# Optimization experiments

Hardware: AMD Instinct MI355X
Metric: run time of the kernel (lower is better)

## Reference

```python
import jax, jax.numpy as jnp
import numpy as np
import math

S, E, D, H = 2048, 1024, 64, 16  # seq, embedding_dim (=D*H), per-head d_model, heads


def setup_inputs() -> dict:
    ks = jax.random.split(jax.random.key(0), 14)
    u = lambda k, sh: jax.random.uniform(k, sh, dtype=jnp.float32)
    n = lambda k, sh, s=0.02: s * jax.random.normal(k, sh, dtype=jnp.float32)
    return {
        "x": jax.random.normal(ks[0], (S, E), dtype=jnp.float32),
        # nn.Parameter(torch.rand(d_model, embedding_dim))
        "Wk": u(ks[1], (D, E)),
        "Wq": u(ks[2], (D, E)),
        "Wv": u(ks[3], (D, E)),
        # per-head Linear(d_model, d_model): weight [out,in]=[D,D], bias [D]
        "hWk": n(ks[4], (H, D, D)), "hbk": n(ks[5], (H, D)),
        "hWv": n(ks[6], (H, D, D)), "hbv": n(ks[7], (H, D)),
        "hWq": n(ks[8], (H, D, D)), "hbq": n(ks[9], (H, D)),
        # last_linear: Linear(D*H, D*H)
        "Wo": n(ks[10], (E, E)), "bo": n(ks[11], (E,)),
        # LayerNorm(D*H)
        "gamma": jnp.ones((E,), jnp.float32),
        "beta": jnp.zeros((E,), jnp.float32),
    }


def reference(x, Wk, Wq, Wv, hWk, hbk, hWv, hbv, hWq, hbq, Wo, bo, gamma, beta):
    # shared projections: [S, E] @ [E, D] -> [S, D]
    K = x @ Wk.T
    Q = x @ Wq.T
    V = x @ Wv.T
    # per-head linears (torch Linear: y = x @ W.T + b), vectorized over heads
    Kh = jnp.einsum('sd,hed->hse', K, hWk) + hbk[:, None, :]  # [H, S, D]
    Vh = jnp.einsum('sd,hed->hse', V, hWv) + hbv[:, None, :]
    Qh = jnp.einsum('sd,hed->hse', Q, hWq) + hbq[:, None, :]
    # scaled dot product attention; scale uses sqrt(d_model)
    scores = jnp.einsum('hqd,hkd->hqk', Qh, Kh) / math.sqrt(D)  # [H, S, S]
    attn = jax.nn.softmax(scores, axis=-1)
    O = jnp.einsum('hqk,hkd->hqd', attn, Vh)  # [H, S, D]
    # concat heads along feature dim (head order) -> [S, H*D]
    cat = jnp.transpose(O, (1, 0, 2)).reshape(S, H * D)
    out = cat @ Wo.T + bo
    # residual + LayerNorm (eps 1e-5)
    y = out + x
    mu = jnp.mean(y, axis=-1, keepdims=True)
    var = jnp.mean(jnp.square(y - mu), axis=-1, keepdims=True)
    return (y - mu) * jax.lax.rsqrt(var + 1e-5) * gamma + beta
```

## Files before the change

kernel.cpp:

```cpp
#include <hip/hip_runtime.h>
#include <math.h>

#define S 2048
#define E 1024
#define D 64
#define H 16

using f16 = _Float16;
typedef _Float16 v8h __attribute__((ext_vector_type(8)));
typedef _Float16 v4h __attribute__((ext_vector_type(4)));
typedef _Float16 v2h __attribute__((ext_vector_type(2)));
typedef float v4f __attribute__((ext_vector_type(4)));

__device__ __forceinline__ float fexp2(float x) { return __builtin_amdgcn_exp2f(x); }

__device__ __forceinline__ void glds16(const f16* g, f16* l) {
    __builtin_amdgcn_global_load_lds(
        (const __attribute__((address_space(1))) void*)g,
        (__attribute__((address_space(3))) void*)l, 16, 0, 0);
}

__global__ void convert_all(const float* __restrict__ x, const float* __restrict__ Wo,
                            f16* __restrict__ Xh, f16* __restrict__ WoB) {
    const size_t i = (size_t)blockIdx.x * 256 + threadIdx.x;
    const size_t NX = (size_t)S * E / 4;
    if (i < NX) {
        v4f w = ((const v4f*)x)[i];
        v4h h = {(f16)w[0], (f16)w[1], (f16)w[2], (f16)w[3]};
        ((v4h*)Xh)[i] = h;
    } else {
        const size_t j = i - NX;
        v4f w = ((const v4f*)Wo)[j];
        v4h h = {(f16)w[0], (f16)w[1], (f16)w[2], (f16)w[3]};
        ((v4h*)WoB)[j] = h;
    }
}

__global__ void wprep(const float* __restrict__ hWk, const float* __restrict__ hWq,
                      const float* __restrict__ hWv,
                      const float* __restrict__ Wk, const float* __restrict__ Wq,
                      const float* __restrict__ Wv,
                      f16* __restrict__ Wc) {
    const int th = blockIdx.x;
    const int type = th >> 4, h = th & 15;
    const int e0 = blockIdx.y * 64;
    const float* hW = ((type == 0) ? hWk : (type == 1) ? hWq : hWv) + (size_t)h * D * D;
    const float* W  = (type == 0) ? Wk : (type == 1) ? Wq : Wv;
    const int t = threadIdx.x;

    __shared__ f16 Ah[64][72];
    __shared__ f16 Bt[64][72];

    {
        const int r16 = t >> 4, c4 = (t & 15) * 4;
#pragma unroll
        for (int rep = 0; rep < 4; ++rep) {
            const int row = rep * 16 + r16;
            v4f a = *(const v4f*)&hW[(size_t)row * D + c4];
#pragma unroll
            for (int j = 0; j < 4; ++j) Ah[row][c4 + j] = (f16)a[j];
            v4f w = *(const v4f*)&W[(size_t)row * E + e0 + c4];
#pragma unroll
            for (int j = 0; j < 4; ++j) Bt[c4 + j][row] = (f16)w[j];
        }
    }
    __syncthreads();

    const int wave = t >> 6, lane = t & 63;
    const int quad = lane >> 4, l16 = lane & 15;
    v4f acc[4] = {{0,0,0,0},{0,0,0,0},{0,0,0,0},{0,0,0,0}};
#pragma unroll
    for (int ks = 0; ks < 2; ++ks) {
        v8h af = *(const v8h*)&Ah[wave * 16 + l16][ks * 32 + quad * 8];
#pragma unroll
        for (int nt = 0; nt < 4; ++nt) {
            v8h bf = *(const v8h*)&Bt[nt * 16 + l16][ks * 32 + quad * 8];
            acc[nt] = __builtin_amdgcn_mfma_f32_16x16x32_f16(af, bf, acc[nt], 0, 0, 0);
        }
    }
#pragma unroll
    for (int r = 0; r < 4; ++r) {
        const int e2 = wave * 16 + quad * 4 + r;
#pragma unroll
        for (int nt = 0; nt < 4; ++nt)
            Wc[((size_t)th * D + e2) * E + e0 + nt * 16 + l16] = (f16)acc[nt][r];
    }
}

__global__ __launch_bounds__(256) void qkv_gemm(
        const f16* __restrict__ Xh, const f16* __restrict__ Wc,
        const float* __restrict__ hbk, const float* __restrict__ hbq,
        const float* __restrict__ hbv,
        f16* __restrict__ Kh, f16* __restrict__ Qh, f16* __restrict__ Vh) {
    const int m0 = blockIdx.x * 128;
    const int n0 = blockIdx.y * 64;
    const int type = n0 >> 10, h = (n0 >> 6) & 15;
    const float* hb = ((type == 0) ? hbk : (type == 1) ? hbq : hbv) + h * D;
    f16* outp = (type == 0) ? Kh : (type == 1) ? Qh : Vh;

    const int t = threadIdx.x;
    const int wave = t >> 6, lane = t & 63;
    const int quad = lane >> 4, l16 = lane & 15;
    const int wm = wave >> 1, wn = wave & 1;

    __shared__ f16 As[128 * 64];
    __shared__ f16 Bs[64 * 64];

    v4f acc[4][2] = {};
    const int lrow8 = lane >> 3, lg = lane & 7;

    for (int k0 = 0; k0 < E; k0 += 64) {
        __syncthreads();
#pragma unroll
        for (int jj = 0; jj < 4; ++jj) {
            const int j = wave * 4 + jj;
            const int row = j * 8 + lrow8;
            const int g = lg ^ (row & 7);
            glds16(Xh + (size_t)(m0 + row) * E + k0 + g * 8, &As[j * 512]);
        }
#pragma unroll
        for (int jj = 0; jj < 2; ++jj) {
            const int j = wave * 2 + jj;
            const int row = j * 8 + lrow8;
            const int g = lg ^ (row & 7);
            glds16(Wc + (size_t)(n0 + row) * E + k0 + g * 8, &Bs[j * 512]);
        }
        __syncthreads();

#pragma unroll
        for (int ks = 0; ks < 2; ++ks) {
            v8h a[4], b[2];
#pragma unroll
            for (int mt = 0; mt < 4; ++mt) {
                const int row = wm * 64 + mt * 16 + l16;
                a[mt] = *(const v8h*)&As[row * 64 + (((ks * 4 + quad) ^ (row & 7)) * 8)];
            }
#pragma unroll
            for (int nt = 0; nt < 2; ++nt) {
                const int row = wn * 32 + nt * 16 + l16;
                b[nt] = *(const v8h*)&Bs[row * 64 + (((ks * 4 + quad) ^ (row & 7)) * 8)];
            }
#pragma unroll
            for (int mt = 0; mt < 4; ++mt)
#pragma unroll
                for (int nt = 0; nt < 2; ++nt)
                    acc[mt][nt] = __builtin_amdgcn_mfma_f32_16x16x32_f16(a[mt], b[nt], acc[mt][nt], 0, 0, 0);
        }
    }

#pragma unroll
    for (int mt = 0; mt < 4; ++mt)
#pragma unroll
        for (int r = 0; r < 4; ++r) {
            const int s = m0 + wm * 64 + mt * 16 + quad * 4 + r;
#pragma unroll
            for (int nt = 0; nt < 2; ++nt) {
                const int d = wn * 32 + nt * 16 + l16;
                outp[((size_t)h * S + s) * D + d] = (f16)(acc[mt][nt][r] + hb[d]);
            }
        }
}

__global__ void v_transpose(const f16* __restrict__ Vh, f16* __restrict__ VhT) {
    const int h = blockIdx.x;
    const int s0 = blockIdx.y * 64;
    const int t = threadIdx.x;

    __shared__ f16 T[64][66];

    {
        const int r = t >> 2, c = (t & 3) * 16;
        v8h a = *(const v8h*)(Vh + ((size_t)h * S + s0 + r) * D + c);
        v8h b = *(const v8h*)(Vh + ((size_t)h * S + s0 + r) * D + c + 8);
#pragma unroll
        for (int j = 0; j < 8; ++j) { T[r][c + j] = a[j]; T[r][c + 8 + j] = b[j]; }
    }
    __syncthreads();
    {
        const int d = t >> 2, sc = (t & 3) * 16;
        v8h a, b;
#pragma unroll
        for (int j = 0; j < 8; ++j) { a[j] = T[sc + j][d]; b[j] = T[sc + 8 + j][d]; }
        f16* o = VhT + ((size_t)h * D + d) * S + s0 + sc;
        *(v8h*)o = a;
        *(v8h*)(o + 8) = b;
    }
}

#define NSPLIT 4
#define KSPAN (S / NSPLIT)
#define ITERS (KSPAN / 64)
#define PPAD 72

__global__ __launch_bounds__(256, 5) void attn_mfma(
        const f16* __restrict__ Qh, const f16* __restrict__ Kh,
        const f16* __restrict__ VhT, f16* __restrict__ Opart,
        float* __restrict__ ml) {
    const int h = blockIdx.y;
    const int q0 = blockIdx.x * 64;
    const int sp = blockIdx.z;
    const int t = threadIdx.x;
    const int wave = t >> 6, lane = t & 63;
    const int quad = lane >> 4, l16 = lane & 15;

    __shared__ f16 Kt[64 * 64];
    __shared__ f16 Vt[80 * 64];
    __shared__ union { f16 P[4][16][PPAD]; f16 O[64][PPAD]; } PO;

    {
        v4h one = {(f16)1, (f16)1, (f16)1, (f16)1};
        *(v4h*)&Vt[64 * 64 + t * 4] = one;
    }

    const int qrow = q0 + wave * 16 + l16;
    v8h qf[2];
    {
        const v8h* qp = (const v8h*)(Qh + ((size_t)h * S + qrow) * D);
        qf[0] = qp[quad];
        qf[1] = qp[quad + 4];
    }

    v4f oc[5] = {};
    float m_run = -INFINITY;
    const float scale = 0.125f * 1.44269504f;
    const int kb = sp * KSPAN;
    const int srow = lane >> 3, sg = lane & 7;

    for (int it = 0; it < ITERS; ++it) {
        __syncthreads();
#pragma unroll
        for (int half = 0; half < 2; ++half) {
            const int row = wave * 16 + half * 8 + srow;
            const int g = sg ^ (row & 7);
            glds16(Kh + ((size_t)h * S + kb + it * 64 + row) * D + g * 8,
                   &Kt[(wave * 16 + half * 8) * 64]);
            glds16(VhT + ((size_t)h * D + row) * S + kb + it * 64 + g * 8,
                   &Vt[(wave * 16 + half * 8) * 64]);
        }
        __syncthreads();

        v4f sc[4] = {};
#pragma unroll
        for (int ks = 0; ks < 2; ++ks)
#pragma unroll
            for (int mt = 0; mt < 4; ++mt) {
                const int key = mt * 16 + l16;
                v8h kf = *(const v8h*)&Kt[key * 64 + (((ks * 4 + quad) ^ (key & 7)) * 8)];
                sc[mt] = __builtin_amdgcn_mfma_f32_16x16x32_f16(kf, qf[ks], sc[mt], 0, 0, 0);
            }

        float v = sc[0][0];
#pragma unroll
        for (int mt = 0; mt < 4; ++mt)
#pragma unroll
            for (int r = 0; r < 4; ++r) v = fmaxf(v, sc[mt][r]);
        v = fmaxf(v, __shfl_xor(v, 16));
        v = fmaxf(v, __shfl_xor(v, 32));
        v *= scale;
        const float mnew = fmaxf(m_run, v);
        const float alpha = fexp2(m_run - mnew);
        m_run = mnew;
#pragma unroll
        for (int i = 0; i < 5; ++i) oc[i] *= alpha;

#pragma unroll
        for (int mt = 0; mt < 4; ++mt) {
            const float p0 = fexp2(fmaf(sc[mt][0], scale, -mnew));
            const float p1 = fexp2(fmaf(sc[mt][1], scale, -mnew));
            const float p2 = fexp2(fmaf(sc[mt][2], scale, -mnew));
            const float p3 = fexp2(fmaf(sc[mt][3], scale, -mnew));
            auto lo = __builtin_amdgcn_cvt_pkrtz(p0, p1);
            auto hi = __builtin_amdgcn_cvt_pkrtz(p2, p3);
            v4h ph; ph[0] = lo[0]; ph[1] = lo[1]; ph[2] = hi[0]; ph[3] = hi[1];
            *(v4h*)&PO.P[wave][l16][mt * 16 + quad * 4] = ph;
        }

#pragma unroll
        for (int ks = 0; ks < 2; ++ks) {
            v8h pf = *(const v8h*)&PO.P[wave][l16][ks * 32 + quad * 8];
#pragma unroll
            for (int mt = 0; mt < 5; ++mt) {
                const int dr = mt * 16 + l16;
                v8h vf = *(const v8h*)&Vt[dr * 64 + (((ks * 4 + quad) ^ (dr & 7)) * 8)];
                oc[mt] = __builtin_amdgcn_mfma_f32_16x16x32_f16(vf, pf, oc[mt], 0, 0, 0);
            }
        }
    }

    const float l = oc[4][0];
    const float invl = 1.f / l;
    __syncthreads();
#pragma unroll
    for (int mt = 0; mt < 4; ++mt) {
        auto lo = __builtin_amdgcn_cvt_pkrtz(oc[mt][0] * invl, oc[mt][1] * invl);
        auto hi = __builtin_amdgcn_cvt_pkrtz(oc[mt][2] * invl, oc[mt][3] * invl);
        v4h oh; oh[0] = lo[0]; oh[1] = lo[1]; oh[2] = hi[0]; oh[3] = hi[1];
        *(v4h*)&PO.O[wave * 16 + l16][mt * 16 + quad * 4] = oh;
    }
    if (quad == 0) {
        float* mlp = ml + (((size_t)sp * H + h) * S + qrow) * 2;
        mlp[0] = m_run;
        mlp[1] = l;
    }
    __syncthreads();
    {
        const int q = t >> 2, dg = (t & 3) * 16;
        v8h o0 = *(const v8h*)&PO.O[q][dg];
        v8h o1 = *(const v8h*)&PO.O[q][dg + 8];
        f16* dst = Opart + (((size_t)sp * H + h) * S + q0 + q) * D + dg;
        *(v8h*)dst = o0;
        *(v8h*)(dst + 8) = o1;
    }
}

__global__ void attn_combine(const f16* __restrict__ Opart,
                             const float* __restrict__ ml,
                             f16* __restrict__ cat) {
    const int q = blockIdx.x;
    const int t = threadIdx.x;
#pragma unroll
    for (int i = 0; i < 4; ++i) {
        const int idx = i * 256 + t;
        const int h = idx >> 6, d = idx & 63;
        float m[NSPLIT], lv[NSPLIT];
        float M = -INFINITY;
#pragma unroll
        for (int sp = 0; sp < NSPLIT; ++sp) {
            const float* mlp = ml + (((size_t)sp * H + h) * S + q) * 2;
            m[sp] = mlp[0]; lv[sp] = mlp[1];
            M = fmaxf(M, m[sp]);
        }
        float asum = 0.f, o = 0.f;
#pragma unroll
        for (int sp = 0; sp < NSPLIT; ++sp) {
            const float a = fexp2(m[sp] - M) * lv[sp];
            asum += a;
            o += a * (float)Opart[(((size_t)sp * H + h) * S + q) * D + d];
        }
        cat[(size_t)q * E + h * D + d] = (f16)(o / asum);
    }
}

__global__ __launch_bounds__(256) void gemm_y(
        const f16* __restrict__ cat, const f16* __restrict__ WoB,
        const float* __restrict__ bo, const float* __restrict__ x,
        float* __restrict__ y) {
    const int m0 = blockIdx.x * 64;
    const int n0 = blockIdx.y * 64;
    const int t = threadIdx.x;
    const int wave = t >> 6, lane = t & 63;
    const int quad = lane >> 4, l16 = lane & 15;
    const int wm = wave >> 1, wn = wave & 1;

    __shared__ f16 As[64 * 64];
    __shared__ f16 Bs[64 * 64];

    v4f acc[2][2] = {};
    const int lrow8 = lane >> 3, lg = lane & 7;

    for (int k0 = 0; k0 < E; k0 += 64) {
        __syncthreads();
#pragma unroll
        for (int jj = 0; jj < 2; ++jj) {
            const int j = wave * 2 + jj;
            const int row = j * 8 + lrow8;
            const int g = lg ^ (row & 7);
            glds16(cat + (size_t)(m0 + row) * E + k0 + g * 8, &As[j * 512]);
            glds16(WoB + (size_t)(n0 + row) * E + k0 + g * 8, &Bs[j * 512]);
        }
        __syncthreads();

#pragma unroll
        for (int ks = 0; ks < 2; ++ks) {
            v8h a[2], b[2];
#pragma unroll
            for (int mt = 0; mt < 2; ++mt) {
                const int row = wm * 32 + mt * 16 + l16;
                a[mt] = *(const v8h*)&As[row * 64 + (((ks * 4 + quad) ^ (row & 7)) * 8)];
            }
#pragma unroll
            for (int nt = 0; nt < 2; ++nt) {
                const int row = wn * 32 + nt * 16 + l16;
                b[nt] = *(const v8h*)&Bs[row * 64 + (((ks * 4 + quad) ^ (row & 7)) * 8)];
            }
#pragma unroll
            for (int mt = 0; mt < 2; ++mt)
#pragma unroll
                for (int nt = 0; nt < 2; ++nt)
                    acc[mt][nt] = __builtin_amdgcn_mfma_f32_16x16x32_f16(a[mt], b[nt], acc[mt][nt], 0, 0, 0);
        }
    }

#pragma unroll
    for (int mt = 0; mt < 2; ++mt)
#pragma unroll
        for (int r = 0; r < 4; ++r) {
            const int m = m0 + wm * 32 + mt * 16 + quad * 4 + r;
#pragma unroll
            for (int nt = 0; nt < 2; ++nt) {
                const int e = n0 + wn * 32 + nt * 16 + l16;
                y[(size_t)m * E + e] = acc[mt][nt][r] + bo[e] + x[(size_t)m * E + e];
            }
        }
}

__global__ void ln(const float* __restrict__ y,
                   const float* __restrict__ gamma,
                   const float* __restrict__ beta,
                   float* __restrict__ out) {
    const int s = blockIdx.x;
    const int t = threadIdx.x;
    __shared__ float red[256];

    v4f yv = *(const v4f*)(y + (size_t)s * E + t * 4);
    red[t] = yv[0] + yv[1] + yv[2] + yv[3];
    __syncthreads();
    for (int w = 128; w > 0; w >>= 1) {
        if (t < w) red[t] += red[t + w];
        __syncthreads();
    }
    const float mu = red[0] * (1.f / E);
    __syncthreads();

    float lv = 0.f;
#pragma unroll
    for (int i = 0; i < 4; ++i) { float dd = yv[i] - mu; lv += dd * dd; }
    red[t] = lv;
    __syncthreads();
    for (int w = 128; w > 0; w >>= 1) {
        if (t < w) red[t] += red[t + w];
        __syncthreads();
    }
    const float rstd = rsqrtf(red[0] * (1.f / E) + 1e-5f);

    v4f o;
#pragma unroll
    for (int i = 0; i < 4; ++i) {
        const int e = t * 4 + i;
        o[i] = (yv[i] - mu) * rstd * gamma[e] + beta[e];
    }
    *(v4f*)(out + (size_t)s * E + t * 4) = o;
}

extern "C" void kernel_launch(void* const* d_in, const int* in_sizes, int n_in,
                              void* d_out, int out_size, void* d_ws, size_t ws_size,
                              hipStream_t stream) {
    const float* x     = (const float*)d_in[0];
    const float* Wk    = (const float*)d_in[1];
    const float* Wq    = (const float*)d_in[2];
    const float* Wv    = (const float*)d_in[3];
    const float* hWk   = (const float*)d_in[4];
    const float* hbk   = (const float*)d_in[5];
    const float* hWv   = (const float*)d_in[6];
    const float* hbv   = (const float*)d_in[7];
    const float* hWq   = (const float*)d_in[8];
    const float* hbq   = (const float*)d_in[9];
    const float* Wo    = (const float*)d_in[10];
    const float* bo    = (const float*)d_in[11];
    const float* gamma = (const float*)d_in[12];
    const float* beta  = (const float*)d_in[13];
    float* out = (float*)d_out;

    char* base = (char*)d_ws;
    const size_t MB = 1u << 20;
    f16*   Kh    = (f16*)(base);
    f16*   Qh    = (f16*)(base + 4 * MB);
    f16*   VhT   = (f16*)(base + 8 * MB);
    f16*   Opart = (f16*)(base + 12 * MB);
    float* ml    = (float*)(base + 28 * MB);
    f16*   WoB   = (f16*)(base + 29 * MB);
    f16*   Xh    = (f16*)(base + 12 * MB);
    f16*   Wc    = (f16*)(base + 16 * MB);
    f16*   Vh    = (f16*)(base + 22 * MB);
    f16*   cat   = (f16*)(base);
    float* y     = (float*)(base + 4 * MB);

    convert_all<<<3072, 256, 0, stream>>>(x, Wo, Xh, WoB);
    wprep<<<dim3(3 * H, E / 64), 256, 0, stream>>>(hWk, hWq, hWv, Wk, Wq, Wv, Wc);
    qkv_gemm<<<dim3(S / 128, 3 * H * D / 64), 256, 0, stream>>>(Xh, Wc, hbk, hbq, hbv,
                                                                Kh, Qh, Vh);
    v_transpose<<<dim3(H, S / 64), 256, 0, stream>>>(Vh, VhT);
    attn_mfma<<<dim3(S / 64, H, NSPLIT), 256, 0, stream>>>(Qh, Kh, VhT, Opart, ml);
    attn_combine<<<S, 256, 0, stream>>>(Opart, ml, cat);
    gemm_y<<<dim3(S / 64, E / 64), 256, 0, stream>>>(cat, WoB, bo, x, y);
    ln<<<S, 256, 0, stream>>>(y, gamma, beta, out);
}
```

Measured before the change: 170.4 us.

## Merge prep kernels and write V transposed directly from QKV GEMM epilogue

Folds the fp16 conversion and the head-weight composition kernels into a single launch that dispatches on block index. Drops the separate V transpose kernel by having the QKV GEMM epilogue store V blocks directly in [h][d][s] layout as 4-wide fp16 vectors. Workspace buffers are moved to non-overlapping regions. This removes two launches and one full round trip of V through memory, at the cost of strided stores in the V epilogue.

```diff
diff --git a/kernel.cpp b/kernel.cpp
--- a/kernel.cpp
+++ b/kernel.cpp
@@ -9,7 +9,6 @@
 using f16 = _Float16;
 typedef _Float16 v8h __attribute__((ext_vector_type(8)));
 typedef _Float16 v4h __attribute__((ext_vector_type(4)));
-typedef _Float16 v2h __attribute__((ext_vector_type(2)));
 typedef float v4f __attribute__((ext_vector_type(4)));
 
 __device__ __forceinline__ float fexp2(float x) { return __builtin_amdgcn_exp2f(x); }
@@ -20,36 +19,39 @@
         (__attribute__((address_space(3))) void*)l, 16, 0, 0);
 }
 
-__global__ void convert_all(const float* __restrict__ x, const float* __restrict__ Wo,
-                            f16* __restrict__ Xh, f16* __restrict__ WoB) {
-    const size_t i = (size_t)blockIdx.x * 256 + threadIdx.x;
-    const size_t NX = (size_t)S * E / 4;
-    if (i < NX) {
-        v4f w = ((const v4f*)x)[i];
-        v4h h = {(f16)w[0], (f16)w[1], (f16)w[2], (f16)w[3]};
-        ((v4h*)Xh)[i] = h;
-    } else {
-        const size_t j = i - NX;
-        v4f w = ((const v4f*)Wo)[j];
-        v4h h = {(f16)w[0], (f16)w[1], (f16)w[2], (f16)w[3]};
-        ((v4h*)WoB)[j] = h;
-    }
-}
-
-__global__ void wprep(const float* __restrict__ hWk, const float* __restrict__ hWq,
-                      const float* __restrict__ hWv,
-                      const float* __restrict__ Wk, const float* __restrict__ Wq,
-                      const float* __restrict__ Wv,
-                      f16* __restrict__ Wc) {
-    const int th = blockIdx.x;
+__global__ void prep(const float* __restrict__ x, const float* __restrict__ Wo,
+                     const float* __restrict__ hWk, const float* __restrict__ hWq,
+                     const float* __restrict__ hWv,
+                     const float* __restrict__ Wk, const float* __restrict__ Wq,
+                     const float* __restrict__ Wv,
+                     f16* __restrict__ Xh, f16* __restrict__ WoB,
+                     f16* __restrict__ Wc) {
+    __shared__ f16 Ah[64][72];
+    __shared__ f16 Bt[64][72];
+    const int t = threadIdx.x;
+
+    if (blockIdx.x < 3072) {
+        const size_t i = (size_t)blockIdx.x * 256 + t;
+        const size_t NX = (size_t)S * E / 4;
+        if (i < NX) {
+            v4f w = ((const v4f*)x)[i];
+            v4h h = {(f16)w[0], (f16)w[1], (f16)w[2], (f16)w[3]};
+            ((v4h*)Xh)[i] = h;
+        } else {
+            const size_t j = i - NX;
+            v4f w = ((const v4f*)Wo)[j];
+            v4h h = {(f16)w[0], (f16)w[1], (f16)w[2], (f16)w[3]};
+            ((v4h*)WoB)[j] = h;
+        }
+        return;
+    }
+
+    const int bb = blockIdx.x - 3072;
+    const int th = bb >> 4;
     const int type = th >> 4, h = th & 15;
-    const int e0 = blockIdx.y * 64;
+    const int e0 = (bb & 15) * 64;
     const float* hW = ((type == 0) ? hWk : (type == 1) ? hWq : hWv) + (size_t)h * D * D;
     const float* W  = (type == 0) ? Wk : (type == 1) ? Wq : Wv;
-    const int t = threadIdx.x;
-
-    __shared__ f16 Ah[64][72];
-    __shared__ f16 Bt[64][72];
 
     {
         const int r16 = t >> 4, c4 = (t & 15) * 4;
@@ -68,7 +70,7 @@
 
     const int wave = t >> 6, lane = t & 63;
     const int quad = lane >> 4, l16 = lane & 15;
-    v4f acc[4] = {{0,0,0,0},{0,0,0,0},{0,0,0,0},{0,0,0,0}};
+    v4f acc[4] = {};
 #pragma unroll
     for (int ks = 0; ks < 2; ++ks) {
         v8h af = *(const v8h*)&Ah[wave * 16 + l16][ks * 32 + quad * 8];
@@ -91,12 +93,11 @@
         const f16* __restrict__ Xh, const f16* __restrict__ Wc,
         const float* __restrict__ hbk, const float* __restrict__ hbq,
         const float* __restrict__ hbv,
-        f16* __restrict__ Kh, f16* __restrict__ Qh, f16* __restrict__ Vh) {
+        f16* __restrict__ Kh, f16* __restrict__ Qh, f16* __restrict__ VhT) {
     const int m0 = blockIdx.x * 128;
     const int n0 = blockIdx.y * 64;
     const int type = n0 >> 10, h = (n0 >> 6) & 15;
     const float* hb = ((type == 0) ? hbk : (type == 1) ? hbq : hbv) + h * D;
-    f16* outp = (type == 0) ? Kh : (type == 1) ? Qh : Vh;
 
     const int t = threadIdx.x;
     const int wave = t >> 6, lane = t & 63;
@@ -148,42 +149,32 @@
         }
     }
 
-#pragma unroll
-    for (int mt = 0; mt < 4; ++mt)
-#pragma unroll
-        for (int r = 0; r < 4; ++r) {
-            const int s = m0 + wm * 64 + mt * 16 + quad * 4 + r;
+    if (type == 2) {
+#pragma unroll
+        for (int mt = 0; mt < 4; ++mt)
 #pragma unroll
             for (int nt = 0; nt < 2; ++nt) {
                 const int d = wn * 32 + nt * 16 + l16;
-                outp[((size_t)h * S + s) * D + d] = (f16)(acc[mt][nt][r] + hb[d]);
-            }
-        }
-}
-
-__global__ void v_transpose(const f16* __restrict__ Vh, f16* __restrict__ VhT) {
-    const int h = blockIdx.x;
-    const int s0 = blockIdx.y * 64;
-    const int t = threadIdx.x;
-
-    __shared__ f16 T[64][66];
-
-    {
-        const int r = t >> 2, c = (t & 3) * 16;
-        v8h a = *(const v8h*)(Vh + ((size_t)h * S + s0 + r) * D + c);
-        v8h b = *(const v8h*)(Vh + ((size_t)h * S + s0 + r) * D + c + 8);
-#pragma unroll
-        for (int j = 0; j < 8; ++j) { T[r][c + j] = a[j]; T[r][c + 8 + j] = b[j]; }
-    }
-    __syncthreads();
-    {
-        const int d = t >> 2, sc = (t & 3) * 16;
-        v8h a, b;
-#pragma unroll
-        for (int j = 0; j < 8; ++j) { a[j] = T[sc + j][d]; b[j] = T[sc + 8 + j][d]; }
-        f16* o = VhT + ((size_t)h * D + d) * S + s0 + sc;
-        *(v8h*)o = a;
-        *(v8h*)(o + 8) = b;
+                const int s = m0 + wm * 64 + mt * 16 + quad * 4;
+                const float b = hb[d];
+                v4h vh;
+#pragma unroll
+                for (int r = 0; r < 4; ++r) vh[r] = (f16)(acc[mt][nt][r] + b);
+                *(v4h*)(VhT + ((size_t)h * D + d) * S + s) = vh;
+            }
+    } else {
+        f16* outp = (type == 0) ? Kh : Qh;
+#pragma unroll
+        for (int mt = 0; mt < 4; ++mt)
+#pragma unroll
+            for (int r = 0; r < 4; ++r) {
+                const int s = m0 + wm * 64 + mt * 16 + quad * 4 + r;
+#pragma unroll
+                for (int nt = 0; nt < 2; ++nt) {
+                    const int d = wn * 32 + nt * 16 + l16;
+                    outp[((size_t)h * S + s) * D + d] = (f16)(acc[mt][nt][r] + hb[d]);
+                }
+            }
     }
 }
 
@@ -469,17 +460,15 @@
     f16*   Opart = (f16*)(base + 12 * MB);
     float* ml    = (float*)(base + 28 * MB);
     f16*   WoB   = (f16*)(base + 29 * MB);
-    f16*   Xh    = (f16*)(base + 12 * MB);
-    f16*   Wc    = (f16*)(base + 16 * MB);
-    f16*   Vh    = (f16*)(base + 22 * MB);
-    f16*   cat   = (f16*)(base);
-    float* y     = (float*)(base + 4 * MB);
-
-    convert_all<<<3072, 256, 0, stream>>>(x, Wo, Xh, WoB);
-    wprep<<<dim3(3 * H, E / 64), 256, 0, stream>>>(hWk, hWq, hWv, Wk, Wq, Wv, Wc);
+    f16*   Xh    = (f16*)(base + 31 * MB);
+    f16*   Wc    = (f16*)(base + 35 * MB);
+    f16*   cat   = (f16*)(base + 41 * MB);
+    float* y     = (float*)(base + 45 * MB);
+
+    prep<<<3072 + 768, 256, 0, stream>>>(x, Wo, hWk, hWq, hWv, Wk, Wq, Wv,
+                                         Xh, WoB, Wc);
     qkv_gemm<<<dim3(S / 128, 3 * H * D / 64), 256, 0, stream>>>(Xh, Wc, hbk, hbq, hbv,
-                                                                Kh, Qh, Vh);
-    v_transpose<<<dim3(H, S / 64), 256, 0, stream>>>(Vh, VhT);
+                                                                Kh, Qh, VhT);
     attn_mfma<<<dim3(S / 64, H, NSPLIT), 256, 0, stream>>>(Qh, Kh, VhT, Opart, ml);
     attn_combine<<<S, 256, 0, stream>>>(Opart, ml, cat);
     gemm_y<<<dim3(S / 64, E / 64), 256, 0, stream>>>(cat, WoB, bo, x, y);
```

Result: faster. 166.9 us (-2.0%).
